# Kernel optimization log

Measured on AMD Instinct MI355X. Metric: run time of the kernel, lower is better.

Reference implementation:

```python
import jax, jax.numpy as jnp
import numpy as np

HIDDEN = 512
HEADS = 8
DHEAD = HIDDEN // HEADS  # 64


def setup_inputs() -> dict:
    key = jax.random.key(0)
    ks = jax.random.split(key, 12)
    B, S = 2, 2048
    inp = {
        "q": jax.random.normal(ks[0], (B, S, HIDDEN), dtype=jnp.float32),
        "k": jax.random.normal(ks[1], (B, S, HIDDEN), dtype=jnp.float32),
        "v": jax.random.normal(ks[2], (B, S, HIDDEN), dtype=jnp.float32),
        "mask": jnp.zeros((B, 1, 1, S), dtype=bool),
    }
    scale = 1.0 / np.sqrt(HIDDEN)
    for i, name in enumerate(["Wq", "Wk", "Wv", "Wm"]):
        inp[name] = jax.random.normal(ks[3 + i], (HIDDEN, HIDDEN), dtype=jnp.float32) * scale
    for i, name in enumerate(["bq", "bk", "bv", "bm"]):
        inp[name] = jax.random.normal(ks[7 + i], (HIDDEN,), dtype=jnp.float32) * 0.01
    return inp


def reference(q, k, v, mask, Wq, Wk, Wv, Wm, bq, bk, bv, bm):
    B = q.shape[0]
    # Linear projections (torch Linear: x @ W.T + b)
    qh = (jnp.einsum("bsd,ed->bse", q, Wq) + bq).reshape(B, HEADS, -1, DHEAD)
    kh = (jnp.einsum("bsd,ed->bse", k, Wk) + bk).reshape(B, HEADS, -1, DHEAD)
    vh = (jnp.einsum("bsd,ed->bse", v, Wv) + bv).reshape(B, HEADS, -1, DHEAD)
    # NOTE: the original module reshapes [B,S,512] -> [B,8,S',64] directly
    # (splitting the sequence dim into heads, not the hidden dim); replicated here.
    s = jnp.einsum("bhqd,bhkd->bhqk", qh, kh) / jnp.sqrt(jnp.float32(DHEAD))
    s = jnp.where(mask, jnp.float32(-1e9), s)
    s = jax.nn.softmax(s, axis=-1)
    # dropout is identity in eval mode
    attn = jnp.einsum("bhqk,bhkd->bhqd", s, vh)  # [B,H,S',64]
    attn = attn.transpose(0, 2, 1, 3).reshape(B, -1, HIDDEN)
    return jnp.einsum("bsd,ed->bse", attn, Wm) + bm
```

## Files before the change

### kernel.cpp

```cpp
#include <hip/hip_runtime.h>
#include <hip/hip_bf16.h>
#include <math.h>

typedef float  f32x4 __attribute__((ext_vector_type(4)));
typedef short  s16x8 __attribute__((ext_vector_type(8)));
typedef short  s16x4 __attribute__((ext_vector_type(4)));
typedef unsigned short u16x4 __attribute__((ext_vector_type(4)));

__device__ inline unsigned short bfc(float f){
  __hip_bfloat16 h = __float2bfloat16(f);
  unsigned short u; __builtin_memcpy(&u, &h, 2); return u;
}

__device__ inline f32x4 mfma16(s16x4 a, s16x4 b, f32x4 c){
#if __has_builtin(__builtin_amdgcn_mfma_f32_16x16x16_bf16)
  return __builtin_amdgcn_mfma_f32_16x16x16_bf16(a, b, c, 0, 0, 0);
#elif __has_builtin(__builtin_amdgcn_mfma_f32_16x16x16bf16_1k)
  return __builtin_amdgcn_mfma_f32_16x16x16bf16_1k(a, b, c, 0, 0, 0);
#else
  asm("v_mfma_f32_16x16x16_bf16 %0, %1, %2, %0" : "+v"(c) : "v"(a), "v"(b));
  return c;
#endif
}

__device__ inline void gl_lds16(const unsigned short* g, unsigned short* l){
  __builtin_amdgcn_global_load_lds(
      (const __attribute__((address_space(1))) unsigned int*)g,
      (__attribute__((address_space(3))) unsigned int*)l, 16, 0, 0);
}

__global__ __launch_bounds__(256) void prep(const float* __restrict__ q, const float* __restrict__ k,
                                            const float* __restrict__ v,
                                            const float* __restrict__ w0, const float* __restrict__ w1,
                                            const float* __restrict__ w2, const float* __restrict__ w3,
                                            const unsigned char* __restrict__ mask,
                                            unsigned short* __restrict__ AP, unsigned short* __restrict__ WP,
                                            float* __restrict__ mf){
  int y = blockIdx.y;
  int t = blockIdx.x * 256 + threadIdx.x;
  if (y < 3){
    const float* src = y==0 ? q : (y==1 ? k : v);
    unsigned short* d = AP + (size_t)y * 2097152;
    int r = t >> 6, g = t & 63;
    const float* sp = src + (size_t)r * 512 + g * 8;
    f32x4 a0 = *(const f32x4*)sp;
    f32x4 a1 = *(const f32x4*)(sp + 4);
    s16x8 o = { (short)bfc(a0.x),(short)bfc(a0.y),(short)bfc(a0.z),(short)bfc(a0.w),
                (short)bfc(a1.x),(short)bfc(a1.y),(short)bfc(a1.z),(short)bfc(a1.w) };
    size_t off = ((size_t)(((r>>4)*16 + (g>>2))*64 + (g&3)*16 + (r&15))) * 8;
    *(s16x8*)(d + off) = o;
  } else if (y < 7){
    if (blockIdx.x < 128){
      int yy = y - 3;
      const float* src = yy==0 ? w0 : yy==1 ? w1 : yy==2 ? w2 : w3;
      int c = t >> 6, g = t & 63;
      const float* sp = src + (size_t)c * 512 + g * 8;
      f32x4 a0 = *(const f32x4*)sp;
      f32x4 a1 = *(const f32x4*)(sp + 4);
      s16x8 o = { (short)bfc(a0.x),(short)bfc(a0.y),(short)bfc(a0.z),(short)bfc(a0.w),
                  (short)bfc(a1.x),(short)bfc(a1.y),(short)bfc(a1.z),(short)bfc(a1.w) };
      size_t off = ((size_t)(((c>>4)*16 + (g>>2))*64 + (g&3)*16 + (c&15))) * 8;
      *(s16x8*)(WP + yy*262144 + off) = o;
    }
  } else if (t < 4096){
    int b = t >> 11, kp = t & 2047;
    int korig = (kp & 255) * 8 + (kp >> 8);
    mf[t] = mask[b*2048 + korig] ? -1.442695e9f : 0.0f;
  }
}

__global__ __launch_bounds__(256) void proj_gemm(const unsigned short* __restrict__ Ap,
    const unsigned short* __restrict__ Wp,
    const float* __restrict__ bq, const float* __restrict__ bk, const float* __restrict__ bv,
    unsigned short* __restrict__ pout, unsigned short* __restrict__ Vtp){
  int z = blockIdx.z;
  const unsigned short* A = Ap + (size_t)z * 2097152;
  const unsigned short* W = Wp + (size_t)z * 262144;
  const float* bias = z==0 ? bq : (z==1 ? bk : bv);

  int w = threadIdx.x >> 6, lane = threadIdx.x & 63;
  int lr = lane & 15, lg = lane >> 4;
  int rt = blockIdx.x * 4 + w;
  int bn = blockIdx.y;

  f32x4 acc[4] = {};
  const unsigned short* Abase = A + ((size_t)rt*8192 + lane*8);
  const unsigned short* Wbase = W + ((size_t)bn*32768 + lane*8);
#pragma unroll 4
  for (int kc = 0; kc < 16; ++kc){
    s16x8 af = *(const s16x8*)(Abase + kc*512);
#pragma unroll
    for (int n = 0; n < 4; ++n){
      s16x8 bf = *(const s16x8*)(Wbase + ((size_t)n*16 + kc)*512);
      acc[n] = __builtin_amdgcn_mfma_f32_16x16x32_bf16(af, bf, acc[n], 0, 0, 0);
    }
  }
  if (z == 0){
    unsigned short* out = pout;
    int orow = rt*16 + lg*4;
#pragma unroll
    for (int n = 0; n < 4; ++n){
      int col = bn*64 + n*16 + lr;
      float bv_ = bias[col];
#pragma unroll
      for (int r = 0; r < 4; ++r)
        out[(size_t)(orow + r)*512 + col] = bfc(acc[n][r] + bv_);
    }
  } else if (z == 1){
    int bh = (rt >> 7) * 8 + ((rt >> 4) & 7);
    unsigned short* kp_ = pout + 2097152 + (size_t)bh*131072;
    int kbase = (rt & 15)*16 + 256*bn;
#pragma unroll
    for (int n = 0; n < 4; ++n){
      int col = bn*64 + n*16 + lr;
      float bv_ = bias[col];
#pragma unroll
      for (int r = 0; r < 4; ++r)
        kp_[(size_t)(kbase + lg*4 + r)*64 + n*16 + lr] = bfc(acc[n][r] + bv_);
    }
  } else {
    int bh = (rt >> 7) * 8 + ((rt >> 4) & 7);
    unsigned short* chunk = Vtp + (size_t)bh*131072 + ((size_t)((rt & 15) + 16*bn))*1024;
#pragma unroll
    for (int n = 0; n < 4; ++n){
      int col = bn*64 + n*16 + lr;
      float bv_ = bias[col];
      u16x4 ov = { bfc(acc[n][0] + bv_), bfc(acc[n][1] + bv_),
                   bfc(acc[n][2] + bv_), bfc(acc[n][3] + bv_) };
      *(u16x4*)(chunk + (n*16 + lr)*16 + lg*4) = ov;
    }
  }
}

__global__ __launch_bounds__(512, 4) void flash(const unsigned short* __restrict__ Pq,
                                             const unsigned short* __restrict__ Kp,
                                             const unsigned short* __restrict__ Vtp,
                                             const float* __restrict__ mf,
                                             unsigned short* __restrict__ aout){
  int qt = blockIdx.x;
  int bh = blockIdx.y;
  int b = bh >> 3, h = bh & 7;
  int w = threadIdx.x >> 6;
  int wq = w & 1, wk = w >> 1;
  int lane = threadIdx.x & 63;
  int lr = lane & 15, lg = lane >> 4;

  const unsigned short* Qh = Pq + (size_t)(b*2048 + h*256)*512;
  const unsigned short* Kh = Kp + (size_t)bh*131072 + (size_t)wk*32768;
  const unsigned short* Vq = Vtp + (size_t)bh*131072 + (size_t)wk*32768;
  const float* mp = mf + b*2048 + wk*512 + lg*4;

  __shared__ char smem[50176];
  unsigned short* ktile = (unsigned short*)smem;
  unsigned short* vtile = (unsigned short*)(smem + 24576);
  float* obuf = (float*)smem;
  float* lbuf = (float*)(smem + 49152);

  int row_l = lane >> 3;
  int cxor  = (lane & 7) ^ row_l;

  unsigned short* kg = const_cast<unsigned short*>(Kh) + (size_t)(8*wq + row_l)*64 + cxor*8;
  unsigned short* vg = const_cast<unsigned short*>(Vq)
                       + (size_t)(wq*8 + row_l + 16*(cxor>>1))*16 + (cxor&1)*8;

  s16x8 qf[2][2];
#pragma unroll
  for (int qq = 0; qq < 2; ++qq){
    int qrow = qt*64 + wq*32 + qq*16 + lr;
    qf[qq][0] = *(const s16x8*)(Qh + (size_t)qrow*64 + lg*8);
    qf[qq][1] = *(const s16x8*)(Qh + (size_t)qrow*64 + 32 + lg*8);
  }

  float l[2] = {0.f, 0.f};
  f32x4 accT[2][4] = {};
  int kswz = (lr & 7) * 16;

#define STAGE(sb) { \
    unsigned short* kd = ktile + ((sb)*4 + wk)*1024; \
    unsigned short* vd = vtile + ((sb)*4 + wk)*1024; \
    gl_lds16(kg, kd + wq*512); \
    gl_lds16(vg, vd + wq*512); \
    kg += 1024; vg += 1024; }

  STAGE(0)
  STAGE(1)
  int cbuf = 0, sbuf = 2;

  for (int t = 0; t < 32; ++t){
    asm volatile("s_waitcnt vmcnt(2)" ::: "memory");
    __builtin_amdgcn_s_barrier();
    __builtin_amdgcn_sched_barrier(0);
    STAGE(sbuf)

    const char* kb = (const char*)(ktile + (cbuf*4 + wk)*1024);
    const char* vb = (const char*)(vtile + (cbuf*4 + wk)*1024);

    s16x8 kf0 = *(const s16x8*)(kb + lr*128 + ((lg*16) ^ kswz));
    s16x8 kf1 = *(const s16x8*)(kb + lr*128 + ((64 + lg*16) ^ kswz));
    f32x4 mv = *(const f32x4*)(mp);
    float s2[2][4];
    __builtin_amdgcn_s_setprio(1);
#pragma unroll
    for (int qq = 0; qq < 2; ++qq){
      f32x4 a = {};
      a = __builtin_amdgcn_mfma_f32_16x16x32_bf16(kf0, qf[qq][0], a, 0, 0, 0);
      a = __builtin_amdgcn_mfma_f32_16x16x32_bf16(kf1, qf[qq][1], a, 0, 0, 0);
#pragma unroll
      for (int r = 0; r < 4; ++r)
        s2[qq][r] = __builtin_fmaf(a[r], 0.18033688f, mv[r]);
    }
    __builtin_amdgcn_s_setprio(0);

    s16x4 pf[2];
#pragma unroll
    for (int qq = 0; qq < 2; ++qq){
      float p0 = __builtin_amdgcn_exp2f(s2[qq][0]);
      float p1 = __builtin_amdgcn_exp2f(s2[qq][1]);
      float p2 = __builtin_amdgcn_exp2f(s2[qq][2]);
      float p3 = __builtin_amdgcn_exp2f(s2[qq][3]);
      l[qq] += (p0 + p1) + (p2 + p3);
      pf[qq] = (s16x4){ (short)bfc(p0), (short)bfc(p1), (short)bfc(p2), (short)bfc(p3) };
    }

    __builtin_amdgcn_s_setprio(1);
#pragma unroll
    for (int nd = 0; nd < 4; ++nd){
      int p = (nd*2 + (lg >> 1)) ^ (lr & 7);
      s16x4 vf = *(const s16x4*)(vb + lr*128 + p*16 + (lg & 1)*8);
      accT[0][nd] = mfma16(vf, pf[0], accT[0][nd]);
      accT[1][nd] = mfma16(vf, pf[1], accT[1][nd]);
    }
    __builtin_amdgcn_s_setprio(0);

    mp += 16;
    cbuf = (cbuf == 2) ? 0 : cbuf + 1;
    sbuf = (sbuf == 2) ? 0 : sbuf + 1;
  }
#undef STAGE

  float lt[2];
#pragma unroll
  for (int qq = 0; qq < 2; ++qq){
    float x = l[qq] + __shfl_xor(l[qq], 16);
    lt[qq] = x + __shfl_xor(x, 32);
  }

  __syncthreads();

  if (wk != 0){
    int j = wk - 1;
#pragma unroll
    for (int qq = 0; qq < 2; ++qq){
      int reg = j*4 + wq*2 + qq;
      if (lg == 0) lbuf[reg*16 + lr] = lt[qq];
#pragma unroll
      for (int nd = 0; nd < 4; ++nd)
        *(f32x4*)&obuf[((size_t)reg*64 + lane)*16 + nd*4] = accT[qq][nd];
    }
  }
  __syncthreads();
  if (wk == 0){
#pragma unroll
    for (int qq = 0; qq < 2; ++qq){
      float ltot = lt[qq];
#pragma unroll
      for (int j = 0; j < 3; ++j)
        ltot += lbuf[(j*4 + wq*2 + qq)*16 + lr];
      float inv = (ltot > 0.f) ? 1.f / ltot : 0.f;
      int q = qt*64 + wq*32 + qq*16 + lr;
      int rt = (b*2048 + q) >> 4;
#pragma unroll
      for (int nd = 0; nd < 4; ++nd){
        f32x4 o = accT[qq][nd];
#pragma unroll
        for (int j = 0; j < 3; ++j){
          int reg = j*4 + wq*2 + qq;
          f32x4 oj = *(const f32x4*)&obuf[((size_t)reg*64 + lane)*16 + nd*4];
          o += oj;
        }
        int g = h*8 + nd*2 + (lg >> 1);
        u16x4 ov = { bfc(o[0]*inv), bfc(o[1]*inv), bfc(o[2]*inv), bfc(o[3]*inv) };
        unsigned short* dp = aout + ((size_t)((rt*16 + (g>>2))*64 + (g&3)*16 + lr))*8 + (lg&1)*4;
        *(u16x4*)dp = ov;
      }
    }
  }
}

__global__ __launch_bounds__(256) void gemm_out(const unsigned short* __restrict__ Ap,
                                                const unsigned short* __restrict__ Wp,
                                                const float* __restrict__ bias,
                                                float* __restrict__ out){
  int w = threadIdx.x >> 6, lane = threadIdx.x & 63;
  int lr = lane & 15, lg = lane >> 4;
  int rt = blockIdx.x * 4 + w;
  int bn = blockIdx.y;
  f32x4 acc[4] = {};
  const unsigned short* Abase = Ap + ((size_t)rt*8192 + lane*8);
  const unsigned short* Wbase = Wp + ((size_t)bn*32768 + lane*8);
#pragma unroll 4
  for (int kc = 0; kc < 16; ++kc){
    s16x8 af = *(const s16x8*)(Abase + kc*512);
#pragma unroll
    for (int n = 0; n < 4; ++n){
      s16x8 bf = *(const s16x8*)(Wbase + ((size_t)n*16 + kc)*512);
      acc[n] = __builtin_amdgcn_mfma_f32_16x16x32_bf16(af, bf, acc[n], 0, 0, 0);
    }
  }
  int orow = rt*16 + lg*4;
#pragma unroll
  for (int n = 0; n < 4; ++n){
    int col = bn*64 + n*16 + lr;
    float bv_ = bias[col];
#pragma unroll
    for (int r = 0; r < 4; ++r)
      out[(size_t)(orow + r)*512 + col] = acc[n][r] + bv_;
  }
}

extern "C" void kernel_launch(void* const* d_in, const int* in_sizes, int n_in,
                              void* d_out, int out_size, void* d_ws, size_t ws_size,
                              hipStream_t stream) {
  const float* q  = (const float*)d_in[0];
  const float* k  = (const float*)d_in[1];
  const float* v  = (const float*)d_in[2];
  const unsigned char* mask = (const unsigned char*)d_in[3];
  const float* Wq = (const float*)d_in[4];
  const float* Wk = (const float*)d_in[5];
  const float* Wv = (const float*)d_in[6];
  const float* Wm = (const float*)d_in[7];
  const float* bq = (const float*)d_in[8];
  const float* bk = (const float*)d_in[9];
  const float* bv = (const float*)d_in[10];
  const float* bm = (const float*)d_in[11];

  unsigned short* ws = (unsigned short*)d_ws;
  unsigned short* WP   = ws;
  float*          MF   = (float*)(ws + 1048576);
  unsigned short* AP   = ws + 1056768;
  unsigned short* PQ   = ws + 7348224;
  unsigned short* VT   = ws + 13639680;
  unsigned short* AO   = ws + 15736832;

  prep<<<dim3(1024, 8), 256, 0, stream>>>(q, k, v, Wq, Wk, Wv, Wm, mask, AP, WP, MF);
  proj_gemm<<<dim3(64, 8, 3), 256, 0, stream>>>(AP, WP, bq, bk, bv, PQ, VT);
  flash<<<dim3(32, 16), 512, 0, stream>>>(PQ, PQ + 2097152, VT, MF, AO);
  gemm_out<<<dim3(64, 8), 256, 0, stream>>>(AO, WP + 3*262144, bm, (float*)d_out);
}
```

Measured before the change: 77.77 us.

## Shrink flash LDS to double buffer and serialize reduction for higher occupancy

```diff
diff --git a/kernel.cpp b/kernel.cpp
--- a/kernel.cpp
+++ b/kernel.cpp
@@ -132,7 +132,7 @@
   }
 }
 
-__global__ __launch_bounds__(512, 4) void flash(const unsigned short* __restrict__ Pq,
+__global__ __launch_bounds__(512, 8) void flash(const unsigned short* __restrict__ Pq,
                                              const unsigned short* __restrict__ Kp,
                                              const unsigned short* __restrict__ Vtp,
                                              const float* __restrict__ mf,
@@ -150,11 +150,11 @@
   const unsigned short* Vq = Vtp + (size_t)bh*131072 + (size_t)wk*32768;
   const float* mp = mf + b*2048 + wk*512 + lg*4;
 
-  __shared__ char smem[50176];
+  __shared__ char smem[32768];
   unsigned short* ktile = (unsigned short*)smem;
-  unsigned short* vtile = (unsigned short*)(smem + 24576);
+  unsigned short* vtile = (unsigned short*)(smem + 16384);
   float* obuf = (float*)smem;
-  float* lbuf = (float*)(smem + 49152);
+  float* lbuf = (float*)(smem + 16384);
 
   int row_l = lane >> 3;
   int cxor  = (lane & 7) ^ row_l;
@@ -183,21 +183,21 @@
     kg += 1024; vg += 1024; }
 
   STAGE(0)
-  STAGE(1)
-  int cbuf = 0, sbuf = 2;
+  f32x4 cmv = *(const f32x4*)(mp);
+  mp += 16;
+  __syncthreads();
+  int cur = 0;
 
   for (int t = 0; t < 32; ++t){
-    asm volatile("s_waitcnt vmcnt(2)" ::: "memory");
-    __builtin_amdgcn_s_barrier();
-    __builtin_amdgcn_sched_barrier(0);
-    STAGE(sbuf)
-
-    const char* kb = (const char*)(ktile + (cbuf*4 + wk)*1024);
-    const char* vb = (const char*)(vtile + (cbuf*4 + wk)*1024);
+    if (t < 31) STAGE(cur ^ 1)
+    f32x4 nmv;
+    if (t < 31){ nmv = *(const f32x4*)(mp); mp += 16; }
+
+    const char* kb = (const char*)(ktile + (cur*4 + wk)*1024);
+    const char* vb = (const char*)(vtile + (cur*4 + wk)*1024);
 
     s16x8 kf0 = *(const s16x8*)(kb + lr*128 + ((lg*16) ^ kswz));
     s16x8 kf1 = *(const s16x8*)(kb + lr*128 + ((64 + lg*16) ^ kswz));
-    f32x4 mv = *(const f32x4*)(mp);
     float s2[2][4];
     __builtin_amdgcn_s_setprio(1);
 #pragma unroll
@@ -207,7 +207,7 @@
       a = __builtin_amdgcn_mfma_f32_16x16x32_bf16(kf1, qf[qq][1], a, 0, 0, 0);
 #pragma unroll
       for (int r = 0; r < 4; ++r)
-        s2[qq][r] = __builtin_fmaf(a[r], 0.18033688f, mv[r]);
+        s2[qq][r] = __builtin_fmaf(a[r], 0.18033688f, cmv[r]);
     }
     __builtin_amdgcn_s_setprio(0);
 
@@ -232,9 +232,9 @@
     }
     __builtin_amdgcn_s_setprio(0);
 
-    mp += 16;
-    cbuf = (cbuf == 2) ? 0 : cbuf + 1;
-    sbuf = (sbuf == 2) ? 0 : sbuf + 1;
+    cmv = nmv;
+    __syncthreads();
+    cur ^= 1;
   }
 #undef STAGE
 
@@ -245,41 +245,44 @@
     lt[qq] = x + __shfl_xor(x, 32);
   }
 
-  __syncthreads();
-
-  if (wk != 0){
-    int j = wk - 1;
+#pragma unroll
+  for (int j = 1; j <= 3; ++j){
+    __syncthreads();
+    if (wk == j){
+#pragma unroll
+      for (int qq = 0; qq < 2; ++qq){
+        int reg = wq*2 + qq;
+        if (lg == 0) lbuf[reg*16 + lr] = lt[qq];
+#pragma unroll
+        for (int nd = 0; nd < 4; ++nd)
+          *(f32x4*)&obuf[((size_t)reg*64 + lane)*16 + nd*4] = accT[qq][nd];
+      }
+    }
+    __syncthreads();
+    if (wk == 0){
+#pragma unroll
+      for (int qq = 0; qq < 2; ++qq){
+        int reg = wq*2 + qq;
+        lt[qq] += lbuf[reg*16 + lr];
+#pragma unroll
+        for (int nd = 0; nd < 4; ++nd){
+          f32x4 oj = *(const f32x4*)&obuf[((size_t)reg*64 + lane)*16 + nd*4];
+          accT[qq][nd] += oj;
+        }
+      }
+    }
+  }
+  if (wk == 0){
 #pragma unroll
     for (int qq = 0; qq < 2; ++qq){
-      int reg = j*4 + wq*2 + qq;
-      if (lg == 0) lbuf[reg*16 + lr] = lt[qq];
-#pragma unroll
-      for (int nd = 0; nd < 4; ++nd)
-        *(f32x4*)&obuf[((size_t)reg*64 + lane)*16 + nd*4] = accT[qq][nd];
-    }
-  }
-  __syncthreads();
-  if (wk == 0){
-#pragma unroll
-    for (int qq = 0; qq < 2; ++qq){
-      float ltot = lt[qq];
-#pragma unroll
-      for (int j = 0; j < 3; ++j)
-        ltot += lbuf[(j*4 + wq*2 + qq)*16 + lr];
-      float inv = (ltot > 0.f) ? 1.f / ltot : 0.f;
+      float inv = (lt[qq] > 0.f) ? 1.f / lt[qq] : 0.f;
       int q = qt*64 + wq*32 + qq*16 + lr;
       int rt = (b*2048 + q) >> 4;
 #pragma unroll
       for (int nd = 0; nd < 4; ++nd){
-        f32x4 o = accT[qq][nd];
-#pragma unroll
-        for (int j = 0; j < 3; ++j){
-          int reg = j*4 + wq*2 + qq;
-          f32x4 oj = *(const f32x4*)&obuf[((size_t)reg*64 + lane)*16 + nd*4];
-          o += oj;
-        }
         int g = h*8 + nd*2 + (lg >> 1);
-        u16x4 ov = { bfc(o[0]*inv), bfc(o[1]*inv), bfc(o[2]*inv), bfc(o[3]*inv) };
+        u16x4 ov = { bfc(accT[qq][nd][0]*inv), bfc(accT[qq][nd][1]*inv),
+                     bfc(accT[qq][nd][2]*inv), bfc(accT[qq][nd][3]*inv) };
         unsigned short* dp = aout + ((size_t)((rt*16 + (g>>2))*64 + (g&3)*16 + lr))*8 + (lg&1)*4;
         *(u16x4*)dp = ov;
       }
```

Result: slower. 228.4 us (+193.7%).
